# Performance work log

Measured on AMD Instinct MI355X. Metric: run time of the kernel, lower is better.

## Reference

```python
import jax, jax.numpy as jnp
import numpy as np

B, N, D, E = 32, 4096, 128, 24576


def setup_inputs() -> dict:
    key = jax.random.key(0)
    k1, k2, k3 = jax.random.split(key, 3)
    x = jax.random.normal(k1, (B, N, D), dtype=jnp.float32)
    edge_index = jax.random.randint(k2, (2, E), 0, N, dtype=jnp.int32)
    # gate_linear: Linear(2*D, 1)
    W = jax.random.normal(k3, (1, 2 * D), dtype=jnp.float32) * 0.05
    b = jnp.zeros((1,), dtype=jnp.float32)
    return {"x": x, "edge_index": edge_index, "W": W, "b": b}


def reference(x, edge_index, W, b):
    # x: [B, N, D]; edge_index: [2, E]
    src, dst = edge_index[0], edge_index[1]
    x_src = x[:, src]              # [B, E, D]
    x_dst = x[:, dst]              # [B, E, D]
    d = x.shape[-1]
    # Linear on concat([x_src, x_dst]) == x_src @ Ws^T + x_dst @ Wd^T + b
    Ws, Wd = W[:, :d], W[:, d:]
    scores = (jnp.einsum('bed,od->beo', x_src, Ws)
              + jnp.einsum('bed,od->beo', x_dst, Wd) + b)  # [B, E, 1]
    attention = jax.nn.sigmoid(scores)
    msg = x_src * attention        # [B, E, D]
    out = jnp.zeros_like(x).at[:, dst].add(msg)  # scatter_add over node axis
    return out
```

## Files before the change

### kernel.cpp

```cpp
#include <hip/hip_runtime.h>


#define NN 4096
#define BB 32
#define DD 128
#define SLOT 32

typedef float f4v __attribute__((ext_vector_type(4)));
typedef unsigned short u16x4 __attribute__((ext_vector_type(4)));

__device__ __forceinline__ unsigned short f2bf(float f) {
    unsigned u = __float_as_uint(f);
    u += 0x7FFF + ((u >> 16) & 1);
    return (unsigned short)(u >> 16);
}
__device__ __forceinline__ float bf2f(unsigned short h) {
    return __uint_as_float(((unsigned)h) << 16);
}

__global__ __launch_bounds__(256) void dots_fill_k(
        const float* __restrict__ x, const float* __restrict__ W,
        const int* __restrict__ src, const int* __restrict__ dst, int E,
        int* __restrict__ deg, int* __restrict__ slots,
        float* __restrict__ dsrc, float* __restrict__ ddst,
        unsigned short* __restrict__ xb16) {
    const int nDotBlocks = BB * NN / 64;
    if (blockIdx.x < nDotBlocks) {
        const int wave = threadIdx.x >> 6;
        const int lane = threadIdx.x & 63;
        const int half = lane >> 5;
        const int l32  = lane & 31;
        const int row0 = blockIdx.x * 64 + wave * 16;
        const float4 ws = *reinterpret_cast<const float4*>(W + l32 * 4);
        const float4 wd = *reinterpret_cast<const float4*>(W + DD + l32 * 4);
#pragma unroll
        for (int i = 0; i < 8; ++i) {
            const int row = row0 + 2 * i + half;
            const float4 v = *reinterpret_cast<const float4*>(x + (size_t)row * DD + l32 * 4);
            u16x4 hv;
            hv.x = f2bf(v.x); hv.y = f2bf(v.y); hv.z = f2bf(v.z); hv.w = f2bf(v.w);
            *reinterpret_cast<u16x4*>(xb16 + (size_t)row * DD + l32 * 4) = hv;
            float ps = v.x * ws.x + v.y * ws.y + v.z * ws.z + v.w * ws.w;
            float pd = v.x * wd.x + v.y * wd.y + v.z * wd.z + v.w * wd.w;
            for (int off = 16; off; off >>= 1) {
                ps += __shfl_xor(ps, off, 64);
                pd += __shfl_xor(pd, off, 64);
            }
            if (l32 == 0) {
                dsrc[row] = ps;
                ddst[row] = pd;
            }
        }
    } else {
        const int e = (blockIdx.x - nDotBlocks) * 256 + threadIdx.x;
        if (e < E) {
            const int d = dst[e];
            const int pos = atomicAdd(&deg[d], 1);
            if (pos < SLOT) slots[d * SLOT + pos] = src[e];
        }
    }
}

__global__ __launch_bounds__(256) void gather_k(const unsigned short* __restrict__ xb16,
                                                const int* __restrict__ deg,
                                                const int* __restrict__ slots,
                                                const float* __restrict__ dsrc,
                                                const float* __restrict__ ddst,
                                                const float* __restrict__ bptr,
                                                float* __restrict__ out) {
    const int sl   = blockIdx.x;
    const int xcd  = sl & 7;
    const int idx  = sl >> 3;
    const int b    = ((idx >> 8) << 3) | xcd;
    const int nblk = idx & 255;
    const int wave = threadIdx.x >> 6;
    const int lane = threadIdx.x & 63;
    const int half = lane >> 5;
    const int l32  = lane & 31;
    const int n0   = nblk * 16 + wave * 4;
    const int nA   = n0 + half;
    const int nB   = n0 + 2 + half;

    const float bias = bptr[0];
    const unsigned short* xb = xb16 + (size_t)b * NN * DD;
    const float* dsb = dsrc + (size_t)b * NN;

    const int4 dv4 = *reinterpret_cast<const int4*>(deg + n0);
    const int cnt0 = dv4.x < SLOT ? dv4.x : SLOT;
    const int cnt1 = dv4.y < SLOT ? dv4.y : SLOT;
    const int cnt2 = dv4.z < SLOT ? dv4.z : SLOT;
    const int cnt3 = dv4.w < SLOT ? dv4.w : SLOT;
    const int cA   = half ? cnt1 : cnt0;
    const int cB   = half ? cnt3 : cnt2;

    const float4 dd4 = *reinterpret_cast<const float4*>(ddst + ((size_t)b << 12) + n0);
    const float sdA = half ? dd4.y : dd4.x;
    const float sdB = half ? dd4.w : dd4.z;

    int   sAl = 0, sBl = 0;
    float aAl = 0.f, aBl = 0.f;
    if (l32 < cA) sAl = slots[nA * SLOT + l32];
    if (l32 < cB) sBl = slots[nB * SLOT + l32];
    if (l32 < cA) {
        const float sc = dsb[sAl] + sdA + bias;
        aAl = 1.0f / (1.0f + __expf(-sc));
    }
    if (l32 < cB) {
        const float sc = dsb[sBl] + sdB + bias;
        aBl = 1.0f / (1.0f + __expf(-sc));
    }

    float4 acc0 = make_float4(0.f, 0.f, 0.f, 0.f);
    float4 acc1 = make_float4(0.f, 0.f, 0.f, 0.f);
    float4 acc2 = make_float4(0.f, 0.f, 0.f, 0.f);
    float4 acc3 = make_float4(0.f, 0.f, 0.f, 0.f);
    const int cmA  = cnt0 > cnt1 ? cnt0 : cnt1;
    const int cmB  = cnt2 > cnt3 ? cnt2 : cnt3;
    const int cmin = cmA < cmB ? cmA : cmB;

    int j = 0;
    for (; j < cmin; j += 2) {
        const int   s0 = __shfl(sAl, j + half, 64);
        const float a0 = __shfl(aAl, j + half, 64);
        const int   s1 = __shfl(sAl, 32 + j + half, 64);
        const float a1 = __shfl(aAl, 32 + j + half, 64);
        const int   s2 = __shfl(sBl, j + half, 64);
        const float a2 = __shfl(aBl, j + half, 64);
        const int   s3 = __shfl(sBl, 32 + j + half, 64);
        const float a3 = __shfl(aBl, 32 + j + half, 64);
        const u16x4 v0 = *reinterpret_cast<const u16x4*>(xb + (size_t)s0 * DD + l32 * 4);
        const u16x4 v1 = *reinterpret_cast<const u16x4*>(xb + (size_t)s1 * DD + l32 * 4);
        const u16x4 v2 = *reinterpret_cast<const u16x4*>(xb + (size_t)s2 * DD + l32 * 4);
        const u16x4 v3 = *reinterpret_cast<const u16x4*>(xb + (size_t)s3 * DD + l32 * 4);
        acc0.x += a0 * bf2f(v0.x); acc0.y += a0 * bf2f(v0.y); acc0.z += a0 * bf2f(v0.z); acc0.w += a0 * bf2f(v0.w);
        acc1.x += a1 * bf2f(v1.x); acc1.y += a1 * bf2f(v1.y); acc1.z += a1 * bf2f(v1.z); acc1.w += a1 * bf2f(v1.w);
        acc2.x += a2 * bf2f(v2.x); acc2.y += a2 * bf2f(v2.y); acc2.z += a2 * bf2f(v2.z); acc2.w += a2 * bf2f(v2.w);
        acc3.x += a3 * bf2f(v3.x); acc3.y += a3 * bf2f(v3.y); acc3.z += a3 * bf2f(v3.z); acc3.w += a3 * bf2f(v3.w);
    }
    for (int jA = j; jA < cmA; jA += 2) {
        const int   s0 = __shfl(sAl, jA + half, 64);
        const float a0 = __shfl(aAl, jA + half, 64);
        const int   s1 = __shfl(sAl, 32 + jA + half, 64);
        const float a1 = __shfl(aAl, 32 + jA + half, 64);
        const u16x4 v0 = *reinterpret_cast<const u16x4*>(xb + (size_t)s0 * DD + l32 * 4);
        const u16x4 v1 = *reinterpret_cast<const u16x4*>(xb + (size_t)s1 * DD + l32 * 4);
        acc0.x += a0 * bf2f(v0.x); acc0.y += a0 * bf2f(v0.y); acc0.z += a0 * bf2f(v0.z); acc0.w += a0 * bf2f(v0.w);
        acc1.x += a1 * bf2f(v1.x); acc1.y += a1 * bf2f(v1.y); acc1.z += a1 * bf2f(v1.z); acc1.w += a1 * bf2f(v1.w);
    }
    for (int jB = j; jB < cmB; jB += 2) {
        const int   s2 = __shfl(sBl, jB + half, 64);
        const float a2 = __shfl(aBl, jB + half, 64);
        const int   s3 = __shfl(sBl, 32 + jB + half, 64);
        const float a3 = __shfl(aBl, 32 + jB + half, 64);
        const u16x4 v2 = *reinterpret_cast<const u16x4*>(xb + (size_t)s2 * DD + l32 * 4);
        const u16x4 v3 = *reinterpret_cast<const u16x4*>(xb + (size_t)s3 * DD + l32 * 4);
        acc2.x += a2 * bf2f(v2.x); acc2.y += a2 * bf2f(v2.y); acc2.z += a2 * bf2f(v2.z); acc2.w += a2 * bf2f(v2.w);
        acc3.x += a3 * bf2f(v3.x); acc3.y += a3 * bf2f(v3.y); acc3.z += a3 * bf2f(v3.z); acc3.w += a3 * bf2f(v3.w);
    }

    acc0.x += __shfl_xor(acc0.x, 32, 64);
    acc0.y += __shfl_xor(acc0.y, 32, 64);
    acc0.z += __shfl_xor(acc0.z, 32, 64);
    acc0.w += __shfl_xor(acc0.w, 32, 64);
    acc1.x += __shfl_xor(acc1.x, 32, 64);
    acc1.y += __shfl_xor(acc1.y, 32, 64);
    acc1.z += __shfl_xor(acc1.z, 32, 64);
    acc1.w += __shfl_xor(acc1.w, 32, 64);
    acc2.x += __shfl_xor(acc2.x, 32, 64);
    acc2.y += __shfl_xor(acc2.y, 32, 64);
    acc2.z += __shfl_xor(acc2.z, 32, 64);
    acc2.w += __shfl_xor(acc2.w, 32, 64);
    acc3.x += __shfl_xor(acc3.x, 32, 64);
    acc3.y += __shfl_xor(acc3.y, 32, 64);
    acc3.z += __shfl_xor(acc3.z, 32, 64);
    acc3.w += __shfl_xor(acc3.w, 32, 64);

    f4v rA, rB;
    rA.x = half ? acc1.x : acc0.x;
    rA.y = half ? acc1.y : acc0.y;
    rA.z = half ? acc1.z : acc0.z;
    rA.w = half ? acc1.w : acc0.w;
    rB.x = half ? acc3.x : acc2.x;
    rB.y = half ? acc3.y : acc2.y;
    rB.z = half ? acc3.z : acc2.z;
    rB.w = half ? acc3.w : acc2.w;
    f4v* pA = reinterpret_cast<f4v*>(out + ((size_t)((b << 12) | nA)) * DD + l32 * 4);
    f4v* pB = reinterpret_cast<f4v*>(out + ((size_t)((b << 12) | nB)) * DD + l32 * 4);
    __builtin_nontemporal_store(rA, pA);
    __builtin_nontemporal_store(rB, pB);
}

extern "C" void kernel_launch(void* const* d_in, const int* in_sizes, int n_in,
                              void* d_out, int out_size, void* d_ws, size_t ws_size,
                              hipStream_t stream) {
    const float* x    = (const float*)d_in[0];
    const int*   ei   = (const int*)d_in[1];
    const float* W    = (const float*)d_in[2];
    const float* bias = (const float*)d_in[3];
    float* out = (float*)d_out;

    const int E = in_sizes[1] / 2;
    const int* src = ei;
    const int* dst = ei + E;

    int* deg     = (int*)d_ws;
    int* slots   = deg + NN;
    float* dsrc  = (float*)(slots + NN * SLOT);
    float* ddst  = dsrc + BB * NN;
    unsigned short* xb16 = (unsigned short*)(ddst + BB * NN);

    hipMemsetAsync(deg, 0, NN * sizeof(int), stream);
    dots_fill_k<<<BB * NN / 64 + (E + 255) / 256, 256, 0, stream>>>(
        x, W, src, dst, E, deg, slots, dsrc, ddst, xb16);
    gather_k<<<BB * NN / 16, 256, 0, stream>>>(xb16, deg, slots, dsrc, ddst, bias, out);
}
```

Baseline: 143.8 us.

## Pack source index into attention low bits and assign one node per 16-lane group

The gather kernel now packs each edge's 12-bit source index into the low mantissa bits of its sigmoid weight, so a single shuffle delivers both values. Each 16-lane quarter-wave owns one destination node and loads 16-byte bf16 vectors (8 elements per lane). This removes the half-wave split, the cross-half shuffle reduction and the separate tail loops. The trade-offs are a slightly perturbed attention weight from truncated mantissa bits, and a loop that runs to the maximum degree rounded up to 4 across all four nodes, with padding entries carrying zero weight.

Result: no change. 142.2 us (-1.1%).

```diff
diff --git a/kernel.cpp b/kernel.cpp
--- a/kernel.cpp
+++ b/kernel.cpp
@@ -7,7 +7,9 @@
 #define SLOT 32
 
 typedef float f4v __attribute__((ext_vector_type(4)));
+typedef float f32x8 __attribute__((ext_vector_type(8)));
 typedef unsigned short u16x4 __attribute__((ext_vector_type(4)));
+typedef unsigned short u16x8 __attribute__((ext_vector_type(8)));
 
 __device__ __forceinline__ unsigned short f2bf(float f) {
     unsigned u = __float_as_uint(f);
@@ -16,6 +18,9 @@
 }
 __device__ __forceinline__ float bf2f(unsigned short h) {
     return __uint_as_float(((unsigned)h) << 16);
+}
+__device__ __forceinline__ float pack_sa(float a, int s) {
+    return __uint_as_float((__float_as_uint(a) & 0xFFFFF000u) | (unsigned)s);
 }
 
 __global__ __launch_bounds__(256) void dots_fill_k(
@@ -77,9 +82,12 @@
     const int lane = threadIdx.x & 63;
     const int half = lane >> 5;
     const int l32  = lane & 31;
+    const int grp1 = (lane >> 4) & 1;
+    const int l16  = lane & 15;
     const int n0   = nblk * 16 + wave * 4;
     const int nA   = n0 + half;
     const int nB   = n0 + 2 + half;
+    const int ng   = n0 + (lane >> 4);
 
     const float bias = bptr[0];
     const unsigned short* xb = xb16 + (size_t)b * NN * DD;
@@ -98,96 +106,52 @@
     const float sdB = half ? dd4.w : dd4.z;
 
     int   sAl = 0, sBl = 0;
-    float aAl = 0.f, aBl = 0.f;
+    float pAl = 0.f, pBl = 0.f;
     if (l32 < cA) sAl = slots[nA * SLOT + l32];
     if (l32 < cB) sBl = slots[nB * SLOT + l32];
     if (l32 < cA) {
         const float sc = dsb[sAl] + sdA + bias;
-        aAl = 1.0f / (1.0f + __expf(-sc));
+        pAl = pack_sa(1.0f / (1.0f + __expf(-sc)), sAl);
     }
     if (l32 < cB) {
         const float sc = dsb[sBl] + sdB + bias;
-        aBl = 1.0f / (1.0f + __expf(-sc));
+        pBl = pack_sa(1.0f / (1.0f + __expf(-sc)), sBl);
     }
 
-    float4 acc0 = make_float4(0.f, 0.f, 0.f, 0.f);
-    float4 acc1 = make_float4(0.f, 0.f, 0.f, 0.f);
-    float4 acc2 = make_float4(0.f, 0.f, 0.f, 0.f);
-    float4 acc3 = make_float4(0.f, 0.f, 0.f, 0.f);
-    const int cmA  = cnt0 > cnt1 ? cnt0 : cnt1;
-    const int cmB  = cnt2 > cnt3 ? cnt2 : cnt3;
-    const int cmin = cmA < cmB ? cmA : cmB;
+    f32x8 acc = {0.f, 0.f, 0.f, 0.f, 0.f, 0.f, 0.f, 0.f};
+    const int cm01 = cnt0 > cnt1 ? cnt0 : cnt1;
+    const int cm23 = cnt2 > cnt3 ? cnt2 : cnt3;
+    const int cmax = cm01 > cm23 ? cm01 : cm23;
+    const int jend = (cmax + 3) & ~3;
+    const int ibase = grp1 << 5;
 
-    int j = 0;
-    for (; j < cmin; j += 2) {
-        const int   s0 = __shfl(sAl, j + half, 64);
-        const float a0 = __shfl(aAl, j + half, 64);
-        const int   s1 = __shfl(sAl, 32 + j + half, 64);
-        const float a1 = __shfl(aAl, 32 + j + half, 64);
-        const int   s2 = __shfl(sBl, j + half, 64);
-        const float a2 = __shfl(aBl, j + half, 64);
-        const int   s3 = __shfl(sBl, 32 + j + half, 64);
-        const float a3 = __shfl(aBl, 32 + j + half, 64);
-        const u16x4 v0 = *reinterpret_cast<const u16x4*>(xb + (size_t)s0 * DD + l32 * 4);
-        const u16x4 v1 = *reinterpret_cast<const u16x4*>(xb + (size_t)s1 * DD + l32 * 4);
-        const u16x4 v2 = *reinterpret_cast<const u16x4*>(xb + (size_t)s2 * DD + l32 * 4);
-        const u16x4 v3 = *reinterpret_cast<const u16x4*>(xb + (size_t)s3 * DD + l32 * 4);
-        acc0.x += a0 * bf2f(v0.x); acc0.y += a0 * bf2f(v0.y); acc0.z += a0 * bf2f(v0.z); acc0.w += a0 * bf2f(v0.w);
-        acc1.x += a1 * bf2f(v1.x); acc1.y += a1 * bf2f(v1.y); acc1.z += a1 * bf2f(v1.z); acc1.w += a1 * bf2f(v1.w);
-        acc2.x += a2 * bf2f(v2.x); acc2.y += a2 * bf2f(v2.y); acc2.z += a2 * bf2f(v2.z); acc2.w += a2 * bf2f(v2.w);
-        acc3.x += a3 * bf2f(v3.x); acc3.y += a3 * bf2f(v3.y); acc3.z += a3 * bf2f(v3.z); acc3.w += a3 * bf2f(v3.w);
-    }
-    for (int jA = j; jA < cmA; jA += 2) {
-        const int   s0 = __shfl(sAl, jA + half, 64);
-        const float a0 = __shfl(aAl, jA + half, 64);
-        const int   s1 = __shfl(sAl, 32 + jA + half, 64);
-        const float a1 = __shfl(aAl, 32 + jA + half, 64);
-        const u16x4 v0 = *reinterpret_cast<const u16x4*>(xb + (size_t)s0 * DD + l32 * 4);
-        const u16x4 v1 = *reinterpret_cast<const u16x4*>(xb + (size_t)s1 * DD + l32 * 4);
-        acc0.x += a0 * bf2f(v0.x); acc0.y += a0 * bf2f(v0.y); acc0.z += a0 * bf2f(v0.z); acc0.w += a0 * bf2f(v0.w);
-        acc1.x += a1 * bf2f(v1.x); acc1.y += a1 * bf2f(v1.y); acc1.z += a1 * bf2f(v1.z); acc1.w += a1 * bf2f(v1.w);
-    }
-    for (int jB = j; jB < cmB; jB += 2) {
-        const int   s2 = __shfl(sBl, jB + half, 64);
-        const float a2 = __shfl(aBl, jB + half, 64);
-        const int   s3 = __shfl(sBl, 32 + jB + half, 64);
-        const float a3 = __shfl(aBl, 32 + jB + half, 64);
-        const u16x4 v2 = *reinterpret_cast<const u16x4*>(xb + (size_t)s2 * DD + l32 * 4);
-        const u16x4 v3 = *reinterpret_cast<const u16x4*>(xb + (size_t)s3 * DD + l32 * 4);
-        acc2.x += a2 * bf2f(v2.x); acc2.y += a2 * bf2f(v2.y); acc2.z += a2 * bf2f(v2.z); acc2.w += a2 * bf2f(v2.w);
-        acc3.x += a3 * bf2f(v3.x); acc3.y += a3 * bf2f(v3.y); acc3.z += a3 * bf2f(v3.z); acc3.w += a3 * bf2f(v3.w);
+#define GBODY(JJ)                                                              \
+    {                                                                          \
+        const unsigned uA = __float_as_uint(__shfl(pAl, ibase | (JJ), 64));    \
+        const unsigned uB = __float_as_uint(__shfl(pBl, ibase | (JJ), 64));    \
+        const unsigned u  = half ? uB : uA;                                    \
+        const int   s = u & 0xFFF;                                             \
+        const float a = __uint_as_float(u);                                    \
+        const u16x8 v = *reinterpret_cast<const u16x8*>(                       \
+            xb + (size_t)s * DD + l16 * 8);                                    \
+        _Pragma("unroll")                                                      \
+        for (int k = 0; k < 8; ++k) acc[k] += a * bf2f(v[k]);                  \
     }
 
-    acc0.x += __shfl_xor(acc0.x, 32, 64);
-    acc0.y += __shfl_xor(acc0.y, 32, 64);
-    acc0.z += __shfl_xor(acc0.z, 32, 64);
-    acc0.w += __shfl_xor(acc0.w, 32, 64);
-    acc1.x += __shfl_xor(acc1.x, 32, 64);
-    acc1.y += __shfl_xor(acc1.y, 32, 64);
-    acc1.z += __shfl_xor(acc1.z, 32, 64);
-    acc1.w += __shfl_xor(acc1.w, 32, 64);
-    acc2.x += __shfl_xor(acc2.x, 32, 64);
-    acc2.y += __shfl_xor(acc2.y, 32, 64);
-    acc2.z += __shfl_xor(acc2.z, 32, 64);
-    acc2.w += __shfl_xor(acc2.w, 32, 64);
-    acc3.x += __shfl_xor(acc3.x, 32, 64);
-    acc3.y += __shfl_xor(acc3.y, 32, 64);
-    acc3.z += __shfl_xor(acc3.z, 32, 64);
-    acc3.w += __shfl_xor(acc3.w, 32, 64);
+    for (int j = 0; j < jend; j += 4) {
+        GBODY(j)
+        GBODY(j + 1)
+        GBODY(j + 2)
+        GBODY(j + 3)
+    }
+#undef GBODY
 
-    f4v rA, rB;
-    rA.x = half ? acc1.x : acc0.x;
-    rA.y = half ? acc1.y : acc0.y;
-    rA.z = half ? acc1.z : acc0.z;
-    rA.w = half ? acc1.w : acc0.w;
-    rB.x = half ? acc3.x : acc2.x;
-    rB.y = half ? acc3.y : acc2.y;
-    rB.z = half ? acc3.z : acc2.z;
-    rB.w = half ? acc3.w : acc2.w;
-    f4v* pA = reinterpret_cast<f4v*>(out + ((size_t)((b << 12) | nA)) * DD + l32 * 4);
-    f4v* pB = reinterpret_cast<f4v*>(out + ((size_t)((b << 12) | nB)) * DD + l32 * 4);
-    __builtin_nontemporal_store(rA, pA);
-    __builtin_nontemporal_store(rB, pB);
+    float* orow = out + ((size_t)((b << 12) | ng)) * DD + l16 * 8;
+    f4v lo, hi;
+    lo.x = acc[0]; lo.y = acc[1]; lo.z = acc[2]; lo.w = acc[3];
+    hi.x = acc[4]; hi.y = acc[5]; hi.z = acc[6]; hi.w = acc[7];
+    __builtin_nontemporal_store(lo, reinterpret_cast<f4v*>(orow));
+    __builtin_nontemporal_store(hi, reinterpret_cast<f4v*>(orow + 4));
 }
 
 extern "C" void kernel_launch(void* const* d_in, const int* in_sizes, int n_in,
```
